# Kernel optimization log

Measured on AMD Instinct MI355X. Metric: run time of the kernel, lower is better.

Reference implementation:

```python
import jax, jax.numpy as jnp
import numpy as np

T, B, I, H = 256, 128, 1024, 1024


def setup_inputs() -> dict:
    key = jax.random.key(0)
    ks = jax.random.split(key, 5)
    # weight init ranges per LSTMLayer.__init__ with wb=0 (no quantization):
    lim_hh = 1.0 / np.sqrt(H)
    lim_ih = 1.0 / np.sqrt(I)
    return {
        "x": jax.random.normal(ks[0], (T, B, I), dtype=jnp.float32),
        "h0": jax.random.normal(ks[1], (B, H), dtype=jnp.float32),
        "c0": jax.random.normal(ks[2], (B, H), dtype=jnp.float32),
        "W_ih": jax.random.uniform(ks[3], (4 * H, I), dtype=jnp.float32, minval=-lim_ih, maxval=lim_ih),
        "W_hh": jax.random.uniform(ks[4], (4 * H, H), dtype=jnp.float32, minval=-lim_hh, maxval=lim_hh),
        "b_ih": jnp.zeros((4 * H,), dtype=jnp.float32),   # uniform_(0, 0)
        "b_hh": jnp.ones((4 * H,), dtype=jnp.float32),    # uniform_(1, 1)
    }


def reference(x, h0, c0, W_ih, W_hh, b_ih, b_hh):
    # Standard LSTM cell, rolled over time with lax.scan.
    # gates layout follows torch LSTMCell: [i, f, g, o] chunks of size H.
    Wih_T = W_ih.T  # [I, 4H]
    Whh_T = W_hh.T  # [H, 4H]
    bias = b_ih + b_hh  # [4H]

    def step(carry, xt):
        h, c = carry  # [B,H] each
        gates = xt @ Wih_T + h @ Whh_T + bias  # [B, 4H]
        i, f, g, o = jnp.split(gates, 4, axis=-1)
        i = jax.nn.sigmoid(i)
        f = jax.nn.sigmoid(f)
        g = jnp.tanh(g)
        o = jax.nn.sigmoid(o)
        c_new = f * c + i * g
        h_new = o * jnp.tanh(c_new)
        return (h_new, c_new), h_new

    (hT, cT), ys = jax.lax.scan(step, (h0, c0), x)
    return ys, hT, cT  # ys: [T, B, H]
```

## Files before the change

kernel.cpp:

```cpp
#include <hip/hip_runtime.h>

#define T_ 256
#define B_ 128
#define I_ 1024
#define H_ 1024
#define G_ 4096
#define BH (B_*H_)
#define TB (T_*B_)

typedef float f32x4 __attribute__((ext_vector_type(4)));
typedef short bf16x8 __attribute__((ext_vector_type(8)));

__device__ inline unsigned short f2bf(float f) {
    union { float f; unsigned int u; } v; v.f = f;
    unsigned int u = v.u;
    unsigned int r = (u + 0x7fffu + ((u >> 16) & 1u)) >> 16;
    return (unsigned short)r;
}
__device__ inline float bf2f(unsigned short s) {
    union { unsigned int u; float f; } v; v.u = ((unsigned int)s) << 16;
    return v.f;
}
__device__ inline float sigmoidf_(float x) { return 1.0f / (1.0f + __expf(-x)); }
__device__ inline float tanhf_(float x) {
    x = fminf(15.0f, fmaxf(-15.0f, x));
    float e = __expf(2.0f * x);
    return (e - 1.0f) / (e + 1.0f);
}

__device__ __forceinline__ void gload16(const unsigned short* g, unsigned short* l) {
    __builtin_amdgcn_global_load_lds(
        (const __attribute__((address_space(1))) void*)g,
        (__attribute__((address_space(3))) void*)l,
        16, 0, 0);
}

__global__ void cvt_kernel(const float* __restrict__ src, unsigned short* __restrict__ dst, int n) {
    int i = (blockIdx.x * blockDim.x + threadIdx.x) * 4;
    int stride = gridDim.x * blockDim.x * 4;
    for (; i < n; i += stride) {
        float4 v = *reinterpret_cast<const float4*>(src + i);
        ushort4 o;
        o.x = f2bf(v.x); o.y = f2bf(v.y); o.z = f2bf(v.z); o.w = f2bf(v.w);
        *reinterpret_cast<ushort4*>(dst + i) = o;
    }
}

__global__ void bias_kernel(const float* __restrict__ a, const float* __restrict__ b, float* __restrict__ out) {
    int i = blockIdx.x * blockDim.x + threadIdx.x;
    if (i < G_) out[i] = a[i] + b[i];
}

__global__ __launch_bounds__(256, 2) void pregemm(
    const unsigned short* __restrict__ xb,
    const unsigned short* __restrict__ wih,
    const float* __restrict__ bias,
    unsigned short* __restrict__ gx)
{
    __shared__ unsigned short Ab[2][128 * 64];
    __shared__ unsigned short Bb[2][128 * 64];

    int swz = (blockIdx.x & 7) * 1024 + (blockIdx.x >> 3);
    int mg = swz & 255;
    int ng = swz >> 8;
    int m0 = mg * 128, n0 = ng * 128;
    int tid = threadIdx.x;
    int w = tid >> 6, l = tid & 63;
    int qm = (w >> 1) * 64, qn = (w & 1) * 64;
    int lr = l & 15, lkidx = (l >> 4);

    int srow = ((w * 4) * 64 + l) >> 3;
    int sk8  = l & 7;

#define STAGE(BUF, KT)                                                              \
    {                                                                               \
        _Pragma("unroll")                                                           \
        for (int it = 0; it < 4; ++it) {                                            \
            int row = srow + it * 8;                                                \
            gload16(xb  + (size_t)(m0 + row) * I_ + (KT) * 64 + sk8 * 8,            \
                    &Ab[BUF][(w * 4 + it) * 512]);                                  \
            gload16(wih + (size_t)(n0 + row) * I_ + (KT) * 64 + sk8 * 8,            \
                    &Bb[BUF][(w * 4 + it) * 512]);                                  \
        }                                                                           \
    }

    f32x4 acc[4][4] = {};
    int buf = 0;
    STAGE(0, 0)
    __syncthreads();

    for (int kt = 0; kt < 16; ++kt) {
        if (kt + 1 < 16) STAGE(buf ^ 1, kt + 1)
        #pragma unroll
        for (int kk = 0; kk < 2; ++kk) {
            bf16x8 a[4], b[4];
            #pragma unroll
            for (int mt = 0; mt < 4; ++mt)
                a[mt] = *reinterpret_cast<const bf16x8*>(
                    &Ab[buf][(qm + mt * 16 + lr) * 64 + kk * 32 + lkidx * 8]);
            #pragma unroll
            for (int nt = 0; nt < 4; ++nt)
                b[nt] = *reinterpret_cast<const bf16x8*>(
                    &Bb[buf][(qn + nt * 16 + lr) * 64 + kk * 32 + lkidx * 8]);
            #pragma unroll
            for (int mt = 0; mt < 4; ++mt)
                #pragma unroll
                for (int nt = 0; nt < 4; ++nt)
                    acc[mt][nt] = __builtin_amdgcn_mfma_f32_16x16x32_bf16(
                        a[mt], b[nt], acc[mt][nt], 0, 0, 0);
        }
        __syncthreads();
        buf ^= 1;
    }
#undef STAGE

    int lq = l >> 4;
    #pragma unroll
    for (int mt = 0; mt < 4; ++mt) {
        #pragma unroll
        for (int nt = 0; nt < 4; ++nt) {
            #pragma unroll
            for (int r = 0; r < 4; ++r) {
                int m = m0 + qm + mt * 16 + lq * 4 + r;
                int n = n0 + qn + nt * 16 + lr;
                gx[(size_t)m * G_ + n] = f2bf(acc[mt][nt][r] + bias[n]);
            }
        }
    }
}

__global__ __launch_bounds__(512) void lstm_recur(
    const unsigned short* __restrict__ whh,
    const unsigned short* __restrict__ gx,
    const float* __restrict__ c0,
    unsigned short* __restrict__ hbuf,
    float* __restrict__ ys,
    float* __restrict__ hT, float* __restrict__ cT,
    unsigned* __restrict__ bar)
{
    __shared__ unsigned short whh_lds[8192 * 8];
    __shared__ float lds_g[4][32][16];

    const int bid = blockIdx.x;
    const int mg  = (bid & 7) >> 1;
    const int ing = (bid >> 3) * 2 + (bid & 1);
    const int m0 = mg * 32, n0 = ing * 16;

    const int tid = threadIdx.x;
    const int w = tid >> 6, l = tid & 63;
    const int mh = w >> 2, kq = w & 3;
    const int lr = l & 15, lkidx = l >> 4;

    const unsigned* pollw = bar + mg * 32 + 2 * kq;
    unsigned* leafw = bar + mg * 32 + (ing >> 3);

    for (int it = 0; it < 16; ++it) {
        int idx = it * 512 + tid;
        int row = idx >> 7;
        int ck  = idx & 127;
        int gg = row >> 4, cc = row & 15;
        bf16x8 v = *reinterpret_cast<const bf16x8*>(
            whh + (size_t)(gg * 1024 + n0 + cc) * H_ + ck * 8);
        *reinterpret_cast<bf16x8*>(whh_lds + ((size_t)ck * 64 + row) * 8) = v;
    }
    __syncthreads();

    const unsigned short* bwave = whh_lds + (((size_t)(kq * 32 + lkidx)) * 64 + lr) * 8;

    const int erow = tid >> 4, ecol = tid & 15;
    const size_t eoff = (size_t)(m0 + erow) * H_ + n0 + ecol;
    float c = c0[eoff];
    const unsigned short* gxp = gx + (size_t)(m0 + erow) * G_ + n0 + ecol;

    const size_t hrow = (size_t)(m0 + mh * 16 + lr) * H_ + kq * 256;

    unsigned short gx0 = gxp[0], gx1 = gxp[1024], gx2 = gxp[2048], gx3 = gxp[3072];

    for (int t = 0; t < T_; ++t) {
        if (t > 0) {
            unsigned tgt = 8u * (unsigned)t;
            while (true) {
                unsigned long long lv;
                asm volatile("global_load_dwordx2 %0, %1, off sc0 sc1"
                             : "=&v"(lv) : "v"(pollw));
                asm volatile("s_waitcnt vmcnt(0)" ::: "memory");
                if ((unsigned)lv >= tgt && (unsigned)(lv >> 32) >= tgt) break;
                __builtin_amdgcn_s_sleep(1);
            }
        }

        const char* hpb = (const char*)hbuf
            + ((size_t)(t & 1) * BH + hrow) * 2 + lkidx * 16;
        bf16x8 hv0, hv1, hv2, hv3, hv4, hv5, hv6, hv7;
        asm volatile("global_load_dwordx4 %0, %1, off sc0 sc1"             : "=&v"(hv0) : "v"(hpb));
        asm volatile("global_load_dwordx4 %0, %1, off offset:64 sc0 sc1"   : "=&v"(hv1) : "v"(hpb));
        asm volatile("global_load_dwordx4 %0, %1, off offset:128 sc0 sc1"  : "=&v"(hv2) : "v"(hpb));
        asm volatile("global_load_dwordx4 %0, %1, off offset:192 sc0 sc1"  : "=&v"(hv3) : "v"(hpb));
        asm volatile("global_load_dwordx4 %0, %1, off offset:256 sc0 sc1"  : "=&v"(hv4) : "v"(hpb));
        asm volatile("global_load_dwordx4 %0, %1, off offset:320 sc0 sc1"  : "=&v"(hv5) : "v"(hpb));
        asm volatile("global_load_dwordx4 %0, %1, off offset:384 sc0 sc1"  : "=&v"(hv6) : "v"(hpb));
        asm volatile("global_load_dwordx4 %0, %1, off offset:448 sc0 sc1"  : "=&v"(hv7) : "v"(hpb));

        {
            float* lg = (float*)lds_g;
            lg[tid] = 0.f; lg[tid + 512] = 0.f; lg[tid + 1024] = 0.f; lg[tid + 1536] = 0.f;
        }

        asm volatile("s_waitcnt vmcnt(0)" ::: "memory");
        __builtin_amdgcn_sched_barrier(0);

        f32x4 acc[4] = {};
#define MFMA_K(KK, HV)                                                              \
        {                                                                           \
            _Pragma("unroll")                                                       \
            for (int g4 = 0; g4 < 4; ++g4) {                                        \
                bf16x8 bb = *reinterpret_cast<const bf16x8*>(                       \
                    bwave + (KK) * 2048 + g4 * 128);                                \
                acc[g4] = __builtin_amdgcn_mfma_f32_16x16x32_bf16(                  \
                    HV, bb, acc[g4], 0, 0, 0);                                      \
            }                                                                       \
        }
        MFMA_K(0, hv0) MFMA_K(1, hv1) MFMA_K(2, hv2) MFMA_K(3, hv3)
        MFMA_K(4, hv4) MFMA_K(5, hv5) MFMA_K(6, hv6) MFMA_K(7, hv7)
#undef MFMA_K
        __syncthreads();

        #pragma unroll
        for (int g4 = 0; g4 < 4; ++g4)
            #pragma unroll
            for (int r = 0; r < 4; ++r)
                atomicAdd(&lds_g[g4][mh * 16 + lkidx * 4 + r][lr], acc[g4][r]);
        __syncthreads();

        float gi = lds_g[0][erow][ecol] + bf2f(gx0);
        float gf = lds_g[1][erow][ecol] + bf2f(gx1);
        float gg = lds_g[2][erow][ecol] + bf2f(gx2);
        float go = lds_g[3][erow][ecol] + bf2f(gx3);
        float iv = sigmoidf_(gi);
        float fv = sigmoidf_(gf);
        float gv = tanhf_(gg);
        float ov = sigmoidf_(go);
        c = fv * c + iv * gv;
        float hn = ov * tanhf_(c);

        unsigned short* hbn = hbuf + (size_t)((t + 1) & 1) * BH;
        float hn_o = __shfl_xor(hn, 1);
        if ((tid & 1) == 0) {
            unsigned u = (unsigned)f2bf(hn) | (((unsigned)f2bf(hn_o)) << 16);
            __hip_atomic_store((unsigned*)(hbn + eoff), u,
                               __ATOMIC_RELAXED, __HIP_MEMORY_SCOPE_AGENT);
        }
        ys[(size_t)t * BH + eoff] = hn;
        if (t == T_ - 1) { hT[eoff] = hn; cT[eoff] = c; }

        if (t + 1 < T_) {
            const unsigned short* p = gxp + (size_t)(t + 1) * B_ * G_;
            gx0 = p[0]; gx1 = p[1024]; gx2 = p[2048]; gx3 = p[3072];
        }

        __syncthreads();

        if (tid == 0 && t + 1 < T_) {
            unsigned one = 1u;
            asm volatile("global_atomic_add %0, %1, off"
                         :: "v"(leafw), "v"(one) : "memory");
        }
    }
}

extern "C" void kernel_launch(void* const* d_in, const int* in_sizes, int n_in,
                              void* d_out, int out_size, void* d_ws, size_t ws_size,
                              hipStream_t stream)
{
    const float* x   = (const float*)d_in[0];
    const float* h0  = (const float*)d_in[1];
    const float* c0  = (const float*)d_in[2];
    const float* Wih = (const float*)d_in[3];
    const float* Whh = (const float*)d_in[4];
    const float* bih = (const float*)d_in[5];
    const float* bhh = (const float*)d_in[6];

    char* ws = (char*)d_ws;
    unsigned short* gx   = (unsigned short*)(ws);
    unsigned short* xb   = (unsigned short*)(ws + 268435456);
    unsigned short* wihb = (unsigned short*)(ws + 335544320);
    unsigned short* whhb = (unsigned short*)(ws + 343932928);
    unsigned short* hbuf = (unsigned short*)(ws + 352321536);
    float*          bias = (float*)(ws + 352845824);
    unsigned*       bar  = (unsigned*)(ws + 352862208);

    float* out = (float*)d_out;
    float* ys = out;
    float* hT = out + (size_t)TB * H_;
    float* cT = hT + BH;

    hipMemsetAsync(bar, 0, 4096, stream);
    cvt_kernel<<<2048, 256, 0, stream>>>(x,   xb,   TB * I_);
    cvt_kernel<<<512,  256, 0, stream>>>(Wih, wihb, G_ * I_);
    cvt_kernel<<<512,  256, 0, stream>>>(Whh, whhb, G_ * H_);
    cvt_kernel<<<128,  256, 0, stream>>>(h0,  hbuf, BH);
    bias_kernel<<<16, 256, 0, stream>>>(bih, bhh, bias);

    pregemm<<<8192, 256, 0, stream>>>(xb, wihb, bias, gx);

    lstm_recur<<<256, 512, 0, stream>>>(whhb, gx, c0, hbuf, ys, hT, cT, bar);
}
```

Baseline: 4.345 ms.

## Replace counter barrier with parity-tagged h data for inter-block sync

Drops the global atomic counter barrier between timesteps. Each bf16 h value now carries a parity tag in its low mantissa bit, so consumers spin on the h loads themselves until every element shows the expected tag. This removes the separate atomic add and poll round trip per step, folding synchronization into the data fetch. In exchange h loses one mantissa bit of precision, and each wave may re-issue the 8 wide loads several times while spinning.

```diff
diff --git a/kernel.cpp b/kernel.cpp
--- a/kernel.cpp
+++ b/kernel.cpp
@@ -10,6 +10,7 @@
 
 typedef float f32x4 __attribute__((ext_vector_type(4)));
 typedef short bf16x8 __attribute__((ext_vector_type(8)));
+typedef int   i32x4  __attribute__((ext_vector_type(4)));
 
 __device__ inline unsigned short f2bf(float f) {
     union { float f; unsigned int u; } v; v.f = f;
@@ -44,6 +45,24 @@
         o.x = f2bf(v.x); o.y = f2bf(v.y); o.z = f2bf(v.z); o.w = f2bf(v.w);
         *reinterpret_cast<ushort4*>(dst + i) = o;
     }
+}
+
+__global__ void cvt_h0_kernel(const float* __restrict__ src, unsigned short* __restrict__ dst, int n) {
+    int i = (blockIdx.x * blockDim.x + threadIdx.x) * 4;
+    int stride = gridDim.x * blockDim.x * 4;
+    for (; i < n; i += stride) {
+        float4 v = *reinterpret_cast<const float4*>(src + i);
+        ushort4 o;
+        o.x = f2bf(v.x) & 0xFFFE; o.y = f2bf(v.y) & 0xFFFE;
+        o.z = f2bf(v.z) & 0xFFFE; o.w = f2bf(v.w) & 0xFFFE;
+        *reinterpret_cast<ushort4*>(dst + i) = o;
+    }
+}
+
+__global__ void init_b1_kernel(unsigned* __restrict__ p) {
+    int i = (blockIdx.x * blockDim.x + threadIdx.x) * 4;
+    i32x4 v = {0x00010001, 0x00010001, 0x00010001, 0x00010001};
+    *reinterpret_cast<i32x4*>(p + i) = v;
 }
 
 __global__ void bias_kernel(const float* __restrict__ a, const float* __restrict__ b, float* __restrict__ out) {
@@ -135,8 +154,7 @@
     const float* __restrict__ c0,
     unsigned short* __restrict__ hbuf,
     float* __restrict__ ys,
-    float* __restrict__ hT, float* __restrict__ cT,
-    unsigned* __restrict__ bar)
+    float* __restrict__ hT, float* __restrict__ cT)
 {
     __shared__ unsigned short whh_lds[8192 * 8];
     __shared__ float lds_g[4][32][16];
@@ -150,9 +168,6 @@
     const int w = tid >> 6, l = tid & 63;
     const int mh = w >> 2, kq = w & 3;
     const int lr = l & 15, lkidx = l >> 4;
-
-    const unsigned* pollw = bar + mg * 32 + 2 * kq;
-    unsigned* leafw = bar + mg * 32 + (ing >> 3);
 
     for (int it = 0; it < 16; ++it) {
         int idx = it * 512 + tid;
@@ -177,47 +192,45 @@
     unsigned short gx0 = gxp[0], gx1 = gxp[1024], gx2 = gxp[2048], gx3 = gxp[3072];
 
     for (int t = 0; t < T_; ++t) {
-        if (t > 0) {
-            unsigned tgt = 8u * (unsigned)t;
-            while (true) {
-                unsigned long long lv;
-                asm volatile("global_load_dwordx2 %0, %1, off sc0 sc1"
-                             : "=&v"(lv) : "v"(pollw));
-                asm volatile("s_waitcnt vmcnt(0)" ::: "memory");
-                if ((unsigned)lv >= tgt && (unsigned)(lv >> 32) >= tgt) break;
-                __builtin_amdgcn_s_sleep(1);
-            }
-        }
-
         const char* hpb = (const char*)hbuf
             + ((size_t)(t & 1) * BH + hrow) * 2 + lkidx * 16;
-        bf16x8 hv0, hv1, hv2, hv3, hv4, hv5, hv6, hv7;
-        asm volatile("global_load_dwordx4 %0, %1, off sc0 sc1"             : "=&v"(hv0) : "v"(hpb));
-        asm volatile("global_load_dwordx4 %0, %1, off offset:64 sc0 sc1"   : "=&v"(hv1) : "v"(hpb));
-        asm volatile("global_load_dwordx4 %0, %1, off offset:128 sc0 sc1"  : "=&v"(hv2) : "v"(hpb));
-        asm volatile("global_load_dwordx4 %0, %1, off offset:192 sc0 sc1"  : "=&v"(hv3) : "v"(hpb));
-        asm volatile("global_load_dwordx4 %0, %1, off offset:256 sc0 sc1"  : "=&v"(hv4) : "v"(hpb));
-        asm volatile("global_load_dwordx4 %0, %1, off offset:320 sc0 sc1"  : "=&v"(hv5) : "v"(hpb));
-        asm volatile("global_load_dwordx4 %0, %1, off offset:384 sc0 sc1"  : "=&v"(hv6) : "v"(hpb));
-        asm volatile("global_load_dwordx4 %0, %1, off offset:448 sc0 sc1"  : "=&v"(hv7) : "v"(hpb));
+        const unsigned expw = ((unsigned)((t >> 1) & 1)) * 0x00010001u;
+        i32x4 hv0, hv1, hv2, hv3, hv4, hv5, hv6, hv7;
+        while (true) {
+            asm volatile("global_load_dwordx4 %0, %1, off sc0 sc1"             : "=&v"(hv0) : "v"(hpb));
+            asm volatile("global_load_dwordx4 %0, %1, off offset:64 sc0 sc1"   : "=&v"(hv1) : "v"(hpb));
+            asm volatile("global_load_dwordx4 %0, %1, off offset:128 sc0 sc1"  : "=&v"(hv2) : "v"(hpb));
+            asm volatile("global_load_dwordx4 %0, %1, off offset:192 sc0 sc1"  : "=&v"(hv3) : "v"(hpb));
+            asm volatile("global_load_dwordx4 %0, %1, off offset:256 sc0 sc1"  : "=&v"(hv4) : "v"(hpb));
+            asm volatile("global_load_dwordx4 %0, %1, off offset:320 sc0 sc1"  : "=&v"(hv5) : "v"(hpb));
+            asm volatile("global_load_dwordx4 %0, %1, off offset:384 sc0 sc1"  : "=&v"(hv6) : "v"(hpb));
+            asm volatile("global_load_dwordx4 %0, %1, off offset:448 sc0 sc1"  : "=&v"(hv7) : "v"(hpb));
+            asm volatile("s_waitcnt vmcnt(0)" ::: "memory");
+            __builtin_amdgcn_sched_barrier(0);
+            unsigned bad = 0;
+#define CHK(HV) bad |= (((unsigned)HV[0] ^ expw) | ((unsigned)HV[1] ^ expw) | \
+                        ((unsigned)HV[2] ^ expw) | ((unsigned)HV[3] ^ expw)) & 0x00010001u;
+            CHK(hv0) CHK(hv1) CHK(hv2) CHK(hv3) CHK(hv4) CHK(hv5) CHK(hv6) CHK(hv7)
+#undef CHK
+            if (__all((int)(bad == 0))) break;
+            __builtin_amdgcn_s_sleep(4);
+        }
 
         {
             float* lg = (float*)lds_g;
             lg[tid] = 0.f; lg[tid + 512] = 0.f; lg[tid + 1024] = 0.f; lg[tid + 1536] = 0.f;
         }
 
-        asm volatile("s_waitcnt vmcnt(0)" ::: "memory");
-        __builtin_amdgcn_sched_barrier(0);
-
         f32x4 acc[4] = {};
 #define MFMA_K(KK, HV)                                                              \
         {                                                                           \
+            bf16x8 av = __builtin_bit_cast(bf16x8, HV);                             \
             _Pragma("unroll")                                                       \
             for (int g4 = 0; g4 < 4; ++g4) {                                        \
                 bf16x8 bb = *reinterpret_cast<const bf16x8*>(                       \
                     bwave + (KK) * 2048 + g4 * 128);                                \
                 acc[g4] = __builtin_amdgcn_mfma_f32_16x16x32_bf16(                  \
-                    HV, bb, acc[g4], 0, 0, 0);                                      \
+                    av, bb, acc[g4], 0, 0, 0);                                      \
             }                                                                       \
         }
         MFMA_K(0, hv0) MFMA_K(1, hv1) MFMA_K(2, hv2) MFMA_K(3, hv3)
@@ -243,12 +256,17 @@
         c = fv * c + iv * gv;
         float hn = ov * tanhf_(c);
 
-        unsigned short* hbn = hbuf + (size_t)((t + 1) & 1) * BH;
-        float hn_o = __shfl_xor(hn, 1);
-        if ((tid & 1) == 0) {
-            unsigned u = (unsigned)f2bf(hn) | (((unsigned)f2bf(hn_o)) << 16);
-            __hip_atomic_store((unsigned*)(hbn + eoff), u,
-                               __ATOMIC_RELAXED, __HIP_MEMORY_SCOPE_AGENT);
+        {
+            const unsigned wtag = ((unsigned)(t + 1) >> 1) & 1u;
+            unsigned us0 = ((unsigned)f2bf(hn) & 0xFFFEu) | wtag;
+            float hn_o = __shfl_xor(hn, 1);
+            unsigned us1 = ((unsigned)f2bf(hn_o) & 0xFFFEu) | wtag;
+            if ((tid & 1) == 0) {
+                unsigned u = us0 | (us1 << 16);
+                unsigned short* hbn = hbuf + (size_t)((t + 1) & 1) * BH;
+                __hip_atomic_store((unsigned*)(hbn + eoff), u,
+                                   __ATOMIC_RELAXED, __HIP_MEMORY_SCOPE_AGENT);
+            }
         }
         ys[(size_t)t * BH + eoff] = hn;
         if (t == T_ - 1) { hT[eoff] = hn; cT[eoff] = c; }
@@ -259,12 +277,6 @@
         }
 
         __syncthreads();
-
-        if (tid == 0 && t + 1 < T_) {
-            unsigned one = 1u;
-            asm volatile("global_atomic_add %0, %1, off"
-                         :: "v"(leafw), "v"(one) : "memory");
-        }
     }
 }
 
@@ -287,21 +299,20 @@
     unsigned short* whhb = (unsigned short*)(ws + 343932928);
     unsigned short* hbuf = (unsigned short*)(ws + 352321536);
     float*          bias = (float*)(ws + 352845824);
-    unsigned*       bar  = (unsigned*)(ws + 352862208);
 
     float* out = (float*)d_out;
     float* ys = out;
     float* hT = out + (size_t)TB * H_;
     float* cT = hT + BH;
 
-    hipMemsetAsync(bar, 0, 4096, stream);
     cvt_kernel<<<2048, 256, 0, stream>>>(x,   xb,   TB * I_);
     cvt_kernel<<<512,  256, 0, stream>>>(Wih, wihb, G_ * I_);
     cvt_kernel<<<512,  256, 0, stream>>>(Whh, whhb, G_ * H_);
-    cvt_kernel<<<128,  256, 0, stream>>>(h0,  hbuf, BH);
+    cvt_h0_kernel<<<128, 256, 0, stream>>>(h0, hbuf, BH);
+    init_b1_kernel<<<64, 256, 0, stream>>>((unsigned*)(hbuf + BH));
     bias_kernel<<<16, 256, 0, stream>>>(bih, bhh, bias);
 
     pregemm<<<8192, 256, 0, stream>>>(xb, wihb, bias, gx);
 
-    lstm_recur<<<256, 512, 0, stream>>>(whhb, gx, c0, hbuf, ys, hT, cT, bar);
-}
+    lstm_recur<<<256, 512, 0, stream>>>(whhb, gx, c0, hbuf, ys, hT, cT);
+}
```

Result: faster. 4.172 ms (-4.0%).
